# Performance work log

Hardware: AMD Instinct MI355X
Metric: run time of the kernel (lower is better)

The kernel has to match this reference:

```python
import jax, jax.numpy as jnp
import numpy as np

N_NODES = 50000
N_EDGES = 800000
D_IN, D_HID, D_OUT = 128, 128, 64


def setup_inputs() -> dict:
    key = jax.random.key(0)
    ks = jax.random.split(key, 8)
    x = jax.random.normal(ks[0], (N_NODES, D_IN), dtype=jnp.float32)
    edge_index = jax.random.randint(ks[1], (2, N_EDGES), 0, N_NODES, dtype=jnp.int64)
    s1 = 1.0 / np.sqrt(D_IN)
    s2 = 1.0 / np.sqrt(D_HID)
    # PyG SAGEConv: out = lin_l(mean_aggr(x_j)) + lin_r(x_root); bias lives in lin_l
    Wl1 = jax.random.uniform(ks[2], (D_HID, D_IN), jnp.float32, -s1, s1)
    bl1 = jnp.zeros((D_HID,), jnp.float32)
    Wr1 = jax.random.uniform(ks[3], (D_HID, D_IN), jnp.float32, -s1, s1)
    Wl2 = jax.random.uniform(ks[4], (D_OUT, D_HID), jnp.float32, -s2, s2)
    bl2 = jnp.zeros((D_OUT,), jnp.float32)
    Wr2 = jax.random.uniform(ks[5], (D_OUT, D_HID), jnp.float32, -s2, s2)
    return {"x": x, "edge_index": edge_index, "Wl1": Wl1, "bl1": bl1, "Wr1": Wr1,
            "Wl2": Wl2, "bl2": bl2, "Wr2": Wr2}


def _sage_conv(x, src, dst, Wl, bl, Wr):
    # mean aggregation of source-node features onto destination nodes
    msg = x[src]                                              # [E, d]
    agg = jax.ops.segment_sum(msg, dst, num_segments=N_NODES)  # [N, d]
    cnt = jax.ops.segment_sum(jnp.ones((src.shape[0],), x.dtype), dst,
                              num_segments=N_NODES)            # [N]
    mean = agg / jnp.maximum(cnt, 1.0)[:, None]
    return mean @ Wl.T + bl + x @ Wr.T


def reference(x, edge_index, Wl1, bl1, Wr1, Wl2, bl2, Wr2):
    src, dst = edge_index[0], edge_index[1]
    h = jax.nn.relu(_sage_conv(x, src, dst, Wl1, bl1, Wr1))
    h = jax.nn.relu(_sage_conv(h, src, dst, Wl2, bl2, Wr2))
    return jax.nn.log_softmax(h, axis=-1)
```

## Files before the change

kernel.cpp:

```cpp
#include <hip/hip_runtime.h>
#include <cstdint>
#include <cstddef>

#define N_NODES 50000
#define N_EDGES 800000
#define ROWS_PAD 50048
#define ZROW 50000
#define BUCKET_CAP 64

typedef _Float16 f16;
typedef _Float16 f16x2 __attribute__((ext_vector_type(2)));
typedef _Float16 f16x8 __attribute__((ext_vector_type(8)));
typedef float f32x2 __attribute__((ext_vector_type(2)));
typedef float f32x4 __attribute__((ext_vector_type(4)));
typedef unsigned short us4 __attribute__((ext_vector_type(4)));


#define NRANGE 16
#define EPT 16
#define CHUNK (256 * EPT)
#define NCHUNK ((N_EDGES + CHUNK - 1) / CHUNK)
#define NB_FILL (NCHUNK * NRANGE)
#define NB_CX 3125
#define NB_CW 192
#define RANGE_SZ (N_NODES / NRANGE)

__global__ __launch_bounds__(256) void preprocess_kernel(
    const int* __restrict__ edge, int* __restrict__ cnt, unsigned short* __restrict__ bucket,
    const float* __restrict__ x, f16* __restrict__ X16, unsigned char* __restrict__ X8,
    unsigned char* __restrict__ H8,
    const float* __restrict__ Wl1, const float* __restrict__ Wr1,
    const float* __restrict__ Wl2, const float* __restrict__ Wr2,
    f16* __restrict__ Wc1, f16* __restrict__ Wc2) {
  const int b = blockIdx.x;
  const int tid = threadIdx.x;
  if (b < NB_FILL) {
    const int r = b & (NRANGE - 1), chunk = b >> 4;
    const int lo = r * RANGE_SZ, hi = lo + RANGE_SZ;
    const int base = chunk * CHUNK + tid;
    #pragma unroll
    for (int i = 0; i < EPT; ++i) {
      const int e = base + i * 256;
      if (e < N_EDGES) {
        const int dst = edge[N_EDGES + e];
        if (dst >= lo && dst < hi) {
          const int src = edge[e];
          const int pos = atomicAdd(&cnt[dst], 1);
          if (pos < BUCKET_CAP) bucket[(size_t)dst * BUCKET_CAP + pos] = (unsigned short)src;
        }
      }
    }
  } else if (b < NB_FILL + NB_CX) {
    const int idx = (b - NB_FILL) * 256 + tid;
    const int row = idx >> 4, c8 = idx & 15;
    const float4 v0 = *reinterpret_cast<const float4*>(x + (size_t)row * 128 + c8 * 8);
    const float4 v1 = *reinterpret_cast<const float4*>(x + (size_t)row * 128 + c8 * 8 + 4);
    f16x8 o;
    o[0] = (f16)v0.x; o[1] = (f16)v0.y; o[2] = (f16)v0.z; o[3] = (f16)v0.w;
    o[4] = (f16)v1.x; o[5] = (f16)v1.y; o[6] = (f16)v1.z; o[7] = (f16)v1.w;
    *reinterpret_cast<f16x8*>(X16 + (size_t)row * 128 + c8 * 8) = o;
    uint2 p;
    int w = __builtin_amdgcn_cvt_pk_fp8_f32(v0.x, v0.y, 0, false);
    w = __builtin_amdgcn_cvt_pk_fp8_f32(v0.z, v0.w, w, true);
    p.x = (unsigned int)w;
    w = __builtin_amdgcn_cvt_pk_fp8_f32(v1.x, v1.y, 0, false);
    w = __builtin_amdgcn_cvt_pk_fp8_f32(v1.z, v1.w, w, true);
    p.y = (unsigned int)w;
    *reinterpret_cast<uint2*>(X8 + (size_t)row * 128 + c8 * 8) = p;
  } else if (b < NB_FILL + NB_CX + NB_CW) {
    const int idx = (b - NB_FILL - NB_CX) * 256 + tid;
    if (idx < 128 * 256) {
      const int n = idx >> 8, k = idx & 255;
      Wc1[idx] = (f16)((k < 128) ? Wl1[n * 128 + k] : Wr1[n * 128 + (k - 128)]);
    } else {
      const int j = idx - 128 * 256;
      const int n = j >> 8, k = j & 255;
      Wc2[j] = (f16)((k < 128) ? Wl2[n * 128 + k] : Wr2[n * 128 + (k - 128)]);
    }
  } else {
    if (tid < 32)
      reinterpret_cast<unsigned int*>(X8 + (size_t)ZROW * 128)[tid] = 0u;
    else if (tid < 64)
      reinterpret_cast<unsigned int*>(H8 + (size_t)ZROW * 128)[tid - 32] = 0u;
  }
}


__device__ __forceinline__ void aggregate_to_lds(
    const unsigned char* __restrict__ F8, const int* __restrict__ cnt,
    const unsigned short* __restrict__ bucket,
    f16 (*M)[136], int wid, int lane) {
  const int quad = lane >> 4, l16 = lane & 15;
  #pragma unroll 1
  for (int g = 0; g < 2; ++g) {
    const int nb = blockIdx.x * 32 + wid * 8 + g * 4;
    const int node = nb + quad;
    const int dv = (lane < 4) ? cnt[nb + lane] : 0;
    const int dq = __shfl(dv, quad, 64);
    const int dqc = min(dq, BUCKET_CAP);
    int md = max(max(__shfl(dv, 0, 64), __shfl(dv, 1, 64)),
                 max(__shfl(dv, 2, 64), __shfl(dv, 3, 64)));
    md = min(md, BUCKET_CAP);
    const us4 b4 = *reinterpret_cast<const us4*>(bucket + (size_t)node * BUCKET_CAP + l16 * 4);
    float acc[8];
    #pragma unroll
    for (int c = 0; c < 8; ++c) acc[c] = 0.f;
    const unsigned char* Fsrc = F8 + l16 * 8;
    for (int j = 0; j < md; j += 16) {
      uint2 v[16];
      #pragma unroll
      for (int k = 0; k < 16; ++k) {
        const int slot = j + k;
        const int idx = __shfl((int)b4[k & 3], quad * 16 + (slot >> 2), 64);
        const int row = (slot < dqc) ? idx : ZROW;
        v[k] = *reinterpret_cast<const uint2*>(Fsrc + (size_t)row * 128);
      }
      #pragma unroll
      for (int k = 0; k < 16; ++k) {
        const f32x2 f0 = __builtin_amdgcn_cvt_pk_f32_fp8((int)v[k].x, false);
        const f32x2 f1 = __builtin_amdgcn_cvt_pk_f32_fp8((int)v[k].x, true);
        const f32x2 f2 = __builtin_amdgcn_cvt_pk_f32_fp8((int)v[k].y, false);
        const f32x2 f3 = __builtin_amdgcn_cvt_pk_f32_fp8((int)v[k].y, true);
        acc[0] += f0[0]; acc[1] += f0[1]; acc[2] += f1[0]; acc[3] += f1[1];
        acc[4] += f2[0]; acc[5] += f2[1]; acc[6] += f3[0]; acc[7] += f3[1];
      }
    }
    const float inv = 1.0f / (float)(dq > 0 ? dq : 1);
    f16x8 o;
    #pragma unroll
    for (int c = 0; c < 8; ++c) o[c] = (f16)(acc[c] * inv);
    *reinterpret_cast<f16x8*>(&M[wid * 8 + g * 4 + quad][l16 * 8]) = o;
  }
}


__global__ __launch_bounds__(256, 4) void layer1_kernel(
    const f16* __restrict__ X16, const unsigned char* __restrict__ X8,
    const int* __restrict__ cnt, const unsigned short* __restrict__ bucket,
    const f16* __restrict__ Wc, const float* __restrict__ bias,
    f16* __restrict__ H16, unsigned char* __restrict__ H8) {
  __shared__ f16 M[32][136];
  const int wid = threadIdx.x >> 6, lane = threadIdx.x & 63;
  const int quad = lane >> 4, l16 = lane & 15;
  aggregate_to_lds(X8, cnt, bucket, M, wid, lane);
  __syncthreads();
  const int rhalf = wid & 1, nhalf = wid >> 1;
  const int row0 = blockIdx.x * 32 + rhalf * 16;
  f32x4 acc[4];
  #pragma unroll
  for (int t = 0; t < 4; ++t) acc[t] = (f32x4){0.f, 0.f, 0.f, 0.f};
  const f16x8* Wb = reinterpret_cast<const f16x8*>(Wc) + quad;
  const f16* Xrow = X16 + (size_t)(row0 + l16) * 128 + quad * 8;
  #pragma unroll
  for (int s = 0; s < 8; ++s) {
    const f16x8 a = (s < 4)
        ? *reinterpret_cast<const f16x8*>(&M[rhalf * 16 + l16][quad * 8 + s * 32])
        : *reinterpret_cast<const f16x8*>(Xrow + (s - 4) * 32);
    #pragma unroll
    for (int t = 0; t < 4; ++t) {
      const int u = nhalf * 4 + t;
      const f16x8 bb = Wb[(u * 16 + l16) * 32 + s * 4];
      acc[t] = __builtin_amdgcn_mfma_f32_16x16x32_f16(a, bb, acc[t], 0, 0, 0);
    }
  }
  #pragma unroll
  for (int t = 0; t < 4; ++t) {
    const int col = (nhalf * 4 + t) * 16 + l16;
    const float bv = bias[col];
    #pragma unroll
    for (int r = 0; r < 4; ++r) {
      const int row = row0 + quad * 4 + r;
      if (row < N_NODES) {
        const float vv = fmaxf(acc[t][r] + bv, 0.f);
        H16[(size_t)row * 128 + col] = (f16)vv;
        const int p = __builtin_amdgcn_cvt_pk_fp8_f32(vv, vv, 0, false);
        H8[(size_t)row * 128 + col] = (unsigned char)(p & 0xFF);
      }
    }
  }
}


__global__ __launch_bounds__(256, 4) void layer2_kernel(
    const f16* __restrict__ H16, const unsigned char* __restrict__ H8,
    const int* __restrict__ cnt, const unsigned short* __restrict__ bucket,
    const f16* __restrict__ Wc, const float* __restrict__ bias,
    float* __restrict__ out) {
  __shared__ f16 M[32][136];
  __shared__ float PM[4][16], PS[4][16];
  const int wid = threadIdx.x >> 6, lane = threadIdx.x & 63;
  const int quad = lane >> 4, l16 = lane & 15;
  aggregate_to_lds(H8, cnt, bucket, M, wid, lane);
  __syncthreads();
  const int rhalf = wid & 1, nhalf = wid >> 1;
  const int row0 = blockIdx.x * 32 + rhalf * 16;
  f32x4 acc[2];
  #pragma unroll
  for (int t = 0; t < 2; ++t) acc[t] = (f32x4){0.f, 0.f, 0.f, 0.f};
  const f16x8* Wb = reinterpret_cast<const f16x8*>(Wc) + quad;
  const f16* Hrow = H16 + (size_t)(row0 + l16) * 128 + quad * 8;
  #pragma unroll
  for (int s = 0; s < 8; ++s) {
    const f16x8 a = (s < 4)
        ? *reinterpret_cast<const f16x8*>(&M[rhalf * 16 + l16][quad * 8 + s * 32])
        : *reinterpret_cast<const f16x8*>(Hrow + (s - 4) * 32);
    #pragma unroll
    for (int t = 0; t < 2; ++t) {
      const int u = nhalf * 2 + t;
      const f16x8 bb = Wb[(u * 16 + l16) * 32 + s * 4];
      acc[t] = __builtin_amdgcn_mfma_f32_16x16x32_f16(a, bb, acc[t], 0, 0, 0);
    }
  }
  float bv[2];
  #pragma unroll
  for (int t = 0; t < 2; ++t) bv[t] = bias[(nhalf * 2 + t) * 16 + l16];
  float v[4][2], pm[4], ps[4];
  #pragma unroll
  for (int r = 0; r < 4; ++r) {
    #pragma unroll
    for (int t = 0; t < 2; ++t) v[r][t] = fmaxf(acc[t][r] + bv[t], 0.f);
    float m = fmaxf(v[r][0], v[r][1]);
    #pragma unroll
    for (int off = 1; off < 16; off <<= 1) m = fmaxf(m, __shfl_xor(m, off, 64));
    float s = __expf(v[r][0] - m) + __expf(v[r][1] - m);
    #pragma unroll
    for (int off = 1; off < 16; off <<= 1) s += __shfl_xor(s, off, 64);
    pm[r] = m;
    ps[r] = s;
  }
  if (l16 == 0) {
    #pragma unroll
    for (int r = 0; r < 4; ++r) {
      PM[wid][quad * 4 + r] = pm[r];
      PS[wid][quad * 4 + r] = ps[r];
    }
  }
  __syncthreads();
  #pragma unroll
  for (int r = 0; r < 4; ++r) {
    const float m2 = PM[wid ^ 2][quad * 4 + r];
    const float s2 = PS[wid ^ 2][quad * 4 + r];
    const float mt = fmaxf(pm[r], m2);
    const float st = ps[r] * __expf(pm[r] - mt) + s2 * __expf(m2 - mt);
    const float ls = mt + __logf(st);
    const int row = row0 + quad * 4 + r;
    if (row < N_NODES) {
      #pragma unroll
      for (int t = 0; t < 2; ++t)
        out[(size_t)row * 64 + (nhalf * 2 + t) * 16 + l16] = v[r][t] - ls;
    }
  }
}


extern "C" void kernel_launch(void* const* d_in, const int* in_sizes, int n_in,
                              void* d_out, int out_size, void* d_ws, size_t ws_size,
                              hipStream_t stream) {
  const float* x   = (const float*)d_in[0];
  const int* edge  = (const int*)d_in[1];
  const float* Wl1 = (const float*)d_in[2];
  const float* bl1 = (const float*)d_in[3];
  const float* Wr1 = (const float*)d_in[4];
  const float* Wl2 = (const float*)d_in[5];
  const float* bl2 = (const float*)d_in[6];
  const float* Wr2 = (const float*)d_in[7];
  float* out = (float*)d_out;

  char* ws = (char*)d_ws;
  size_t off = 0;
  auto alloc = [&](size_t bytes) -> char* {
    char* p = ws + off;
    off = (off + bytes + 255) & ~(size_t)255;
    return p;
  };
  int* cnt               = (int*)alloc((size_t)ROWS_PAD * 4);
  unsigned short* bucket = (unsigned short*)alloc((size_t)ROWS_PAD * BUCKET_CAP * 2);
  f16* X16           = (f16*)alloc((size_t)ROWS_PAD * 128 * 2);
  f16* H16           = (f16*)alloc((size_t)ROWS_PAD * 128 * 2);
  unsigned char* X8  = (unsigned char*)alloc((size_t)ROWS_PAD * 128);
  unsigned char* H8  = (unsigned char*)alloc((size_t)ROWS_PAD * 128);
  f16* Wc1           = (f16*)alloc((size_t)128 * 256 * 2);
  f16* Wc2           = (f16*)alloc((size_t)64 * 256 * 2);

  hipMemsetAsync(cnt, 0, (size_t)ROWS_PAD * 4, stream);

  preprocess_kernel<<<NB_FILL + NB_CX + NB_CW + 1, 256, 0, stream>>>(
      edge, cnt, bucket, x, X16, X8, H8, Wl1, Wr1, Wl2, Wr2, Wc1, Wc2);

  layer1_kernel<<<ROWS_PAD / 32, 256, 0, stream>>>(X16, X8, cnt, bucket, Wc1, bl1, H16, H8);
  layer2_kernel<<<ROWS_PAD / 32, 256, 0, stream>>>(H16, H8, cnt, bucket, Wc2, bl2, out);
}
```

Measured before the change: 216.7 us.

## Halve rows per block in layer kernels and use nontemporal preprocessing loads

Layer kernels now handle 16 nodes per block instead of 32. Each wave aggregates a single group of 4 nodes, and the MFMA work is split across the four waves by output column tiles, with the layer-2 log-softmax reduced over all four waves. This doubles the grid so there are more independent blocks to hide gather latency and to spread the tail. The cost is more blocks and reloading the weight tiles per block. Preprocessing also switches edge and x loads and the X16/X8 stores to nontemporal builtins to avoid polluting the cache.

After: 232.8 us. 1.07x slower.

```diff
diff --git a/kernel.cpp b/kernel.cpp
--- a/kernel.cpp
+++ b/kernel.cpp
@@ -13,6 +13,8 @@
 typedef _Float16 f16x8 __attribute__((ext_vector_type(8)));
 typedef float f32x2 __attribute__((ext_vector_type(2)));
 typedef float f32x4 __attribute__((ext_vector_type(4)));
+typedef float fx4 __attribute__((ext_vector_type(4)));
+typedef unsigned int u32x2 __attribute__((ext_vector_type(2)));
 typedef unsigned short us4 __attribute__((ext_vector_type(4)));
 
 
@@ -42,9 +44,9 @@
     for (int i = 0; i < EPT; ++i) {
       const int e = base + i * 256;
       if (e < N_EDGES) {
-        const int dst = edge[N_EDGES + e];
+        const int dst = __builtin_nontemporal_load(edge + N_EDGES + e);
         if (dst >= lo && dst < hi) {
-          const int src = edge[e];
+          const int src = __builtin_nontemporal_load(edge + e);
           const int pos = atomicAdd(&cnt[dst], 1);
           if (pos < BUCKET_CAP) bucket[(size_t)dst * BUCKET_CAP + pos] = (unsigned short)src;
         }
@@ -53,20 +55,22 @@
   } else if (b < NB_FILL + NB_CX) {
     const int idx = (b - NB_FILL) * 256 + tid;
     const int row = idx >> 4, c8 = idx & 15;
-    const float4 v0 = *reinterpret_cast<const float4*>(x + (size_t)row * 128 + c8 * 8);
-    const float4 v1 = *reinterpret_cast<const float4*>(x + (size_t)row * 128 + c8 * 8 + 4);
+    const fx4 v0 =
+        __builtin_nontemporal_load(reinterpret_cast<const fx4*>(x + (size_t)row * 128 + c8 * 8));
+    const fx4 v1 = __builtin_nontemporal_load(
+        reinterpret_cast<const fx4*>(x + (size_t)row * 128 + c8 * 8 + 4));
     f16x8 o;
-    o[0] = (f16)v0.x; o[1] = (f16)v0.y; o[2] = (f16)v0.z; o[3] = (f16)v0.w;
-    o[4] = (f16)v1.x; o[5] = (f16)v1.y; o[6] = (f16)v1.z; o[7] = (f16)v1.w;
-    *reinterpret_cast<f16x8*>(X16 + (size_t)row * 128 + c8 * 8) = o;
-    uint2 p;
-    int w = __builtin_amdgcn_cvt_pk_fp8_f32(v0.x, v0.y, 0, false);
-    w = __builtin_amdgcn_cvt_pk_fp8_f32(v0.z, v0.w, w, true);
-    p.x = (unsigned int)w;
-    w = __builtin_amdgcn_cvt_pk_fp8_f32(v1.x, v1.y, 0, false);
-    w = __builtin_amdgcn_cvt_pk_fp8_f32(v1.z, v1.w, w, true);
-    p.y = (unsigned int)w;
-    *reinterpret_cast<uint2*>(X8 + (size_t)row * 128 + c8 * 8) = p;
+    o[0] = (f16)v0[0]; o[1] = (f16)v0[1]; o[2] = (f16)v0[2]; o[3] = (f16)v0[3];
+    o[4] = (f16)v1[0]; o[5] = (f16)v1[1]; o[6] = (f16)v1[2]; o[7] = (f16)v1[3];
+    __builtin_nontemporal_store(o, reinterpret_cast<f16x8*>(X16 + (size_t)row * 128 + c8 * 8));
+    u32x2 p;
+    int w = __builtin_amdgcn_cvt_pk_fp8_f32(v0[0], v0[1], 0, false);
+    w = __builtin_amdgcn_cvt_pk_fp8_f32(v0[2], v0[3], w, true);
+    p[0] = (unsigned int)w;
+    w = __builtin_amdgcn_cvt_pk_fp8_f32(v1[0], v1[1], 0, false);
+    w = __builtin_amdgcn_cvt_pk_fp8_f32(v1[2], v1[3], w, true);
+    p[1] = (unsigned int)w;
+    __builtin_nontemporal_store(p, reinterpret_cast<u32x2*>(X8 + (size_t)row * 128 + c8 * 8));
   } else if (b < NB_FILL + NB_CX + NB_CW) {
     const int idx = (b - NB_FILL - NB_CX) * 256 + tid;
     if (idx < 128 * 256) {
@@ -86,51 +90,48 @@
 }
 
 
-__device__ __forceinline__ void aggregate_to_lds(
+__device__ __forceinline__ void aggregate4_to_lds(
     const unsigned char* __restrict__ F8, const int* __restrict__ cnt,
     const unsigned short* __restrict__ bucket,
     f16 (*M)[136], int wid, int lane) {
   const int quad = lane >> 4, l16 = lane & 15;
-  #pragma unroll 1
-  for (int g = 0; g < 2; ++g) {
-    const int nb = blockIdx.x * 32 + wid * 8 + g * 4;
-    const int node = nb + quad;
-    const int dv = (lane < 4) ? cnt[nb + lane] : 0;
-    const int dq = __shfl(dv, quad, 64);
-    const int dqc = min(dq, BUCKET_CAP);
-    int md = max(max(__shfl(dv, 0, 64), __shfl(dv, 1, 64)),
-                 max(__shfl(dv, 2, 64), __shfl(dv, 3, 64)));
-    md = min(md, BUCKET_CAP);
-    const us4 b4 = *reinterpret_cast<const us4*>(bucket + (size_t)node * BUCKET_CAP + l16 * 4);
-    float acc[8];
-    #pragma unroll
-    for (int c = 0; c < 8; ++c) acc[c] = 0.f;
-    const unsigned char* Fsrc = F8 + l16 * 8;
-    for (int j = 0; j < md; j += 16) {
-      uint2 v[16];
-      #pragma unroll
-      for (int k = 0; k < 16; ++k) {
-        const int slot = j + k;
-        const int idx = __shfl((int)b4[k & 3], quad * 16 + (slot >> 2), 64);
-        const int row = (slot < dqc) ? idx : ZROW;
-        v[k] = *reinterpret_cast<const uint2*>(Fsrc + (size_t)row * 128);
-      }
-      #pragma unroll
-      for (int k = 0; k < 16; ++k) {
-        const f32x2 f0 = __builtin_amdgcn_cvt_pk_f32_fp8((int)v[k].x, false);
-        const f32x2 f1 = __builtin_amdgcn_cvt_pk_f32_fp8((int)v[k].x, true);
-        const f32x2 f2 = __builtin_amdgcn_cvt_pk_f32_fp8((int)v[k].y, false);
-        const f32x2 f3 = __builtin_amdgcn_cvt_pk_f32_fp8((int)v[k].y, true);
-        acc[0] += f0[0]; acc[1] += f0[1]; acc[2] += f1[0]; acc[3] += f1[1];
-        acc[4] += f2[0]; acc[5] += f2[1]; acc[6] += f3[0]; acc[7] += f3[1];
-      }
-    }
-    const float inv = 1.0f / (float)(dq > 0 ? dq : 1);
-    f16x8 o;
-    #pragma unroll
-    for (int c = 0; c < 8; ++c) o[c] = (f16)(acc[c] * inv);
-    *reinterpret_cast<f16x8*>(&M[wid * 8 + g * 4 + quad][l16 * 8]) = o;
-  }
+  const int nb = blockIdx.x * 16 + wid * 4;
+  const int node = nb + quad;
+  const int dv = (lane < 4) ? cnt[nb + lane] : 0;
+  const int dq = __shfl(dv, quad, 64);
+  const int dqc = min(dq, BUCKET_CAP);
+  int md = max(max(__shfl(dv, 0, 64), __shfl(dv, 1, 64)),
+               max(__shfl(dv, 2, 64), __shfl(dv, 3, 64)));
+  md = min(md, BUCKET_CAP);
+  const us4 b4 = *reinterpret_cast<const us4*>(bucket + (size_t)node * BUCKET_CAP + l16 * 4);
+  float acc[8];
+  #pragma unroll
+  for (int c = 0; c < 8; ++c) acc[c] = 0.f;
+  const unsigned char* Fsrc = F8 + l16 * 8;
+  for (int j = 0; j < md; j += 16) {
+    u32x2 v[16];
+    #pragma unroll
+    for (int k = 0; k < 16; ++k) {
+      const int slot = j + k;
+      const int idx = __shfl((int)b4[k & 3], quad * 16 + (slot >> 2), 64);
+      const int row = (slot < dqc) ? idx : ZROW;
+      v[k] = *reinterpret_cast<const u32x2*>(Fsrc + (size_t)row * 128);
+    }
+    #pragma unroll
+    for (int k = 0; k < 16; ++k) {
+      const f32x2 f0 = __builtin_amdgcn_cvt_pk_f32_fp8((int)v[k][0], false);
+      const f32x2 f1 = __builtin_amdgcn_cvt_pk_f32_fp8((int)v[k][0], true);
+      const f32x2 f2 = __builtin_amdgcn_cvt_pk_f32_fp8((int)v[k][1], false);
+      const f32x2 f3 = __builtin_amdgcn_cvt_pk_f32_fp8((int)v[k][1], true);
+      acc[0] += f0[0]; acc[1] += f0[1]; acc[2] += f1[0]; acc[3] += f1[1];
+      acc[4] += f2[0]; acc[5] += f2[1]; acc[6] += f3[0]; acc[7] += f3[1];
+    }
+  }
+  const float inv = 1.0f / (float)(dq > 0 ? dq : 1);
+  f16x8 o;
+  #pragma unroll
+  for (int c = 0; c < 8; ++c) o[c] = (f16)(acc[c] * inv);
+  *reinterpret_cast<f16x8*>(&M[wid * 4 + quad][l16 * 8]) = o;
 }
 
 
@@ -139,33 +140,32 @@
     const int* __restrict__ cnt, const unsigned short* __restrict__ bucket,
     const f16* __restrict__ Wc, const float* __restrict__ bias,
     f16* __restrict__ H16, unsigned char* __restrict__ H8) {
-  __shared__ f16 M[32][136];
+  __shared__ f16 M[16][136];
   const int wid = threadIdx.x >> 6, lane = threadIdx.x & 63;
   const int quad = lane >> 4, l16 = lane & 15;
-  aggregate_to_lds(X8, cnt, bucket, M, wid, lane);
+  aggregate4_to_lds(X8, cnt, bucket, M, wid, lane);
   __syncthreads();
-  const int rhalf = wid & 1, nhalf = wid >> 1;
-  const int row0 = blockIdx.x * 32 + rhalf * 16;
-  f32x4 acc[4];
-  #pragma unroll
-  for (int t = 0; t < 4; ++t) acc[t] = (f32x4){0.f, 0.f, 0.f, 0.f};
+  const int row0 = blockIdx.x * 16;
+  f32x4 acc[2];
+  #pragma unroll
+  for (int t = 0; t < 2; ++t) acc[t] = (f32x4){0.f, 0.f, 0.f, 0.f};
   const f16x8* Wb = reinterpret_cast<const f16x8*>(Wc) + quad;
   const f16* Xrow = X16 + (size_t)(row0 + l16) * 128 + quad * 8;
   #pragma unroll
   for (int s = 0; s < 8; ++s) {
     const f16x8 a = (s < 4)
-        ? *reinterpret_cast<const f16x8*>(&M[rhalf * 16 + l16][quad * 8 + s * 32])
+        ? *reinterpret_cast<const f16x8*>(&M[l16][quad * 8 + s * 32])
         : *reinterpret_cast<const f16x8*>(Xrow + (s - 4) * 32);
     #pragma unroll
-    for (int t = 0; t < 4; ++t) {
-      const int u = nhalf * 4 + t;
+    for (int t = 0; t < 2; ++t) {
+      const int u = wid * 2 + t;
       const f16x8 bb = Wb[(u * 16 + l16) * 32 + s * 4];
       acc[t] = __builtin_amdgcn_mfma_f32_16x16x32_f16(a, bb, acc[t], 0, 0, 0);
     }
   }
   #pragma unroll
-  for (int t = 0; t < 4; ++t) {
-    const int col = (nhalf * 4 + t) * 16 + l16;
+  for (int t = 0; t < 2; ++t) {
+    const int col = (wid * 2 + t) * 16 + l16;
     const float bv = bias[col];
     #pragma unroll
     for (int r = 0; r < 4; ++r) {
@@ -186,43 +186,33 @@
     const int* __restrict__ cnt, const unsigned short* __restrict__ bucket,
     const f16* __restrict__ Wc, const float* __restrict__ bias,
     float* __restrict__ out) {
-  __shared__ f16 M[32][136];
+  __shared__ f16 M[16][136];
   __shared__ float PM[4][16], PS[4][16];
   const int wid = threadIdx.x >> 6, lane = threadIdx.x & 63;
   const int quad = lane >> 4, l16 = lane & 15;
-  aggregate_to_lds(H8, cnt, bucket, M, wid, lane);
+  aggregate4_to_lds(H8, cnt, bucket, M, wid, lane);
   __syncthreads();
-  const int rhalf = wid & 1, nhalf = wid >> 1;
-  const int row0 = blockIdx.x * 32 + rhalf * 16;
-  f32x4 acc[2];
-  #pragma unroll
-  for (int t = 0; t < 2; ++t) acc[t] = (f32x4){0.f, 0.f, 0.f, 0.f};
+  const int row0 = blockIdx.x * 16;
+  f32x4 acc = (f32x4){0.f, 0.f, 0.f, 0.f};
   const f16x8* Wb = reinterpret_cast<const f16x8*>(Wc) + quad;
   const f16* Hrow = H16 + (size_t)(row0 + l16) * 128 + quad * 8;
   #pragma unroll
   for (int s = 0; s < 8; ++s) {
     const f16x8 a = (s < 4)
-        ? *reinterpret_cast<const f16x8*>(&M[rhalf * 16 + l16][quad * 8 + s * 32])
+        ? *reinterpret_cast<const f16x8*>(&M[l16][quad * 8 + s * 32])
         : *reinterpret_cast<const f16x8*>(Hrow + (s - 4) * 32);
-    #pragma unroll
-    for (int t = 0; t < 2; ++t) {
-      const int u = nhalf * 2 + t;
-      const f16x8 bb = Wb[(u * 16 + l16) * 32 + s * 4];
-      acc[t] = __builtin_amdgcn_mfma_f32_16x16x32_f16(a, bb, acc[t], 0, 0, 0);
-    }
-  }
-  float bv[2];
-  #pragma unroll
-  for (int t = 0; t < 2; ++t) bv[t] = bias[(nhalf * 2 + t) * 16 + l16];
-  float v[4][2], pm[4], ps[4];
+    const f16x8 bb = Wb[(wid * 16 + l16) * 32 + s * 4];
+    acc = __builtin_amdgcn_mfma_f32_16x16x32_f16(a, bb, acc, 0, 0, 0);
+  }
+  const float bv = bias[wid * 16 + l16];
+  float v[4], pm[4], ps[4];
   #pragma unroll
   for (int r = 0; r < 4; ++r) {
-    #pragma unroll
-    for (int t = 0; t < 2; ++t) v[r][t] = fmaxf(acc[t][r] + bv[t], 0.f);
-    float m = fmaxf(v[r][0], v[r][1]);
+    v[r] = fmaxf(acc[r] + bv, 0.f);
+    float m = v[r];
     #pragma unroll
     for (int off = 1; off < 16; off <<= 1) m = fmaxf(m, __shfl_xor(m, off, 64));
-    float s = __expf(v[r][0] - m) + __expf(v[r][1] - m);
+    float s = __expf(v[r] - m);
     #pragma unroll
     for (int off = 1; off < 16; off <<= 1) s += __shfl_xor(s, off, 64);
     pm[r] = m;
@@ -238,17 +228,15 @@
   __syncthreads();
   #pragma unroll
   for (int r = 0; r < 4; ++r) {
-    const float m2 = PM[wid ^ 2][quad * 4 + r];
-    const float s2 = PS[wid ^ 2][quad * 4 + r];
-    const float mt = fmaxf(pm[r], m2);
-    const float st = ps[r] * __expf(pm[r] - mt) + s2 * __expf(m2 - mt);
+    const int idx = quad * 4 + r;
+    const float m0 = PM[0][idx], m1 = PM[1][idx], m2 = PM[2][idx], m3 = PM[3][idx];
+    const float mt = fmaxf(fmaxf(m0, m1), fmaxf(m2, m3));
+    const float st = PS[0][idx] * __expf(m0 - mt) + PS[1][idx] * __expf(m1 - mt) +
+                     PS[2][idx] * __expf(m2 - mt) + PS[3][idx] * __expf(m3 - mt);
     const float ls = mt + __logf(st);
-    const int row = row0 + quad * 4 + r;
-    if (row < N_NODES) {
-      #pragma unroll
-      for (int t = 0; t < 2; ++t)
-        out[(size_t)row * 64 + (nhalf * 2 + t) * 16 + l16] = v[r][t] - ls;
-    }
+    const int row = row0 + idx;
+    if (row < N_NODES)
+      out[(size_t)row * 64 + wid * 16 + l16] = v[r] - ls;
   }
 }
 
@@ -287,6 +275,6 @@
   preprocess_kernel<<<NB_FILL + NB_CX + NB_CW + 1, 256, 0, stream>>>(
       edge, cnt, bucket, x, X16, X8, H8, Wl1, Wr1, Wl2, Wr2, Wc1, Wc2);
 
-  layer1_kernel<<<ROWS_PAD / 32, 256, 0, stream>>>(X16, X8, cnt, bucket, Wc1, bl1, H16, H8);
-  layer2_kernel<<<ROWS_PAD / 32, 256, 0, stream>>>(H16, H8, cnt, bucket, Wc2, bl2, out);
-}
+  layer1_kernel<<<ROWS_PAD / 16, 256, 0, stream>>>(X16, X8, cnt, bucket, Wc1, bl1, H16, H8);
+  layer2_kernel<<<ROWS_PAD / 16, 256, 0, stream>>>(H16, H8, cnt, bucket, Wc2, bl2, out);
+}
```

## Drop fp16 feature copies and read root features from fp8 buffers

Applied to the files above, without the earlier changes.

Removes the X16 and H16 half-precision copies, so the root-term operand of each layer's MFMA is loaded from the existing fp8 buffers and decoded in registers. The root-row loads are issued before aggregation so they overlap with the gather. The aggregation gather loop is unrolled to 32 outstanding loads instead of 16. This cuts global write and read traffic for the fp16 copies. In exchange the root term loses precision (fp8 instead of fp16) and register pressure rises from the larger gather unroll.

Result: slower. 232.5 us (+7.3%).

```diff
diff --git a/kernel.cpp b/kernel.cpp
--- a/kernel.cpp
+++ b/kernel.cpp
@@ -13,6 +13,8 @@
 typedef _Float16 f16x8 __attribute__((ext_vector_type(8)));
 typedef float f32x2 __attribute__((ext_vector_type(2)));
 typedef float f32x4 __attribute__((ext_vector_type(4)));
+typedef float fx4 __attribute__((ext_vector_type(4)));
+typedef unsigned int u32x2 __attribute__((ext_vector_type(2)));
 typedef unsigned short us4 __attribute__((ext_vector_type(4)));
 
 
@@ -27,8 +29,7 @@
 
 __global__ __launch_bounds__(256) void preprocess_kernel(
     const int* __restrict__ edge, int* __restrict__ cnt, unsigned short* __restrict__ bucket,
-    const float* __restrict__ x, f16* __restrict__ X16, unsigned char* __restrict__ X8,
-    unsigned char* __restrict__ H8,
+    const float* __restrict__ x, unsigned char* __restrict__ X8, unsigned char* __restrict__ H8,
     const float* __restrict__ Wl1, const float* __restrict__ Wr1,
     const float* __restrict__ Wl2, const float* __restrict__ Wr2,
     f16* __restrict__ Wc1, f16* __restrict__ Wc2) {
@@ -53,20 +54,16 @@
   } else if (b < NB_FILL + NB_CX) {
     const int idx = (b - NB_FILL) * 256 + tid;
     const int row = idx >> 4, c8 = idx & 15;
-    const float4 v0 = *reinterpret_cast<const float4*>(x + (size_t)row * 128 + c8 * 8);
-    const float4 v1 = *reinterpret_cast<const float4*>(x + (size_t)row * 128 + c8 * 8 + 4);
-    f16x8 o;
-    o[0] = (f16)v0.x; o[1] = (f16)v0.y; o[2] = (f16)v0.z; o[3] = (f16)v0.w;
-    o[4] = (f16)v1.x; o[5] = (f16)v1.y; o[6] = (f16)v1.z; o[7] = (f16)v1.w;
-    *reinterpret_cast<f16x8*>(X16 + (size_t)row * 128 + c8 * 8) = o;
-    uint2 p;
-    int w = __builtin_amdgcn_cvt_pk_fp8_f32(v0.x, v0.y, 0, false);
-    w = __builtin_amdgcn_cvt_pk_fp8_f32(v0.z, v0.w, w, true);
-    p.x = (unsigned int)w;
-    w = __builtin_amdgcn_cvt_pk_fp8_f32(v1.x, v1.y, 0, false);
-    w = __builtin_amdgcn_cvt_pk_fp8_f32(v1.z, v1.w, w, true);
-    p.y = (unsigned int)w;
-    *reinterpret_cast<uint2*>(X8 + (size_t)row * 128 + c8 * 8) = p;
+    const fx4 v0 = *reinterpret_cast<const fx4*>(x + (size_t)row * 128 + c8 * 8);
+    const fx4 v1 = *reinterpret_cast<const fx4*>(x + (size_t)row * 128 + c8 * 8 + 4);
+    u32x2 p;
+    int w = __builtin_amdgcn_cvt_pk_fp8_f32(v0[0], v0[1], 0, false);
+    w = __builtin_amdgcn_cvt_pk_fp8_f32(v0[2], v0[3], w, true);
+    p[0] = (unsigned int)w;
+    w = __builtin_amdgcn_cvt_pk_fp8_f32(v1[0], v1[1], 0, false);
+    w = __builtin_amdgcn_cvt_pk_fp8_f32(v1[2], v1[3], w, true);
+    p[1] = (unsigned int)w;
+    *reinterpret_cast<u32x2*>(X8 + (size_t)row * 128 + c8 * 8) = p;
   } else if (b < NB_FILL + NB_CX + NB_CW) {
     const int idx = (b - NB_FILL - NB_CX) * 256 + tid;
     if (idx < 128 * 256) {
@@ -83,6 +80,17 @@
     else if (tid < 64)
       reinterpret_cast<unsigned int*>(H8 + (size_t)ZROW * 128)[tid - 32] = 0u;
   }
+}
+
+__device__ __forceinline__ f16x8 decode8(u32x2 v) {
+  const f32x2 f0 = __builtin_amdgcn_cvt_pk_f32_fp8((int)v[0], false);
+  const f32x2 f1 = __builtin_amdgcn_cvt_pk_f32_fp8((int)v[0], true);
+  const f32x2 f2 = __builtin_amdgcn_cvt_pk_f32_fp8((int)v[1], false);
+  const f32x2 f3 = __builtin_amdgcn_cvt_pk_f32_fp8((int)v[1], true);
+  f16x8 a;
+  a[0] = (f16)f0[0]; a[1] = (f16)f0[1]; a[2] = (f16)f1[0]; a[3] = (f16)f1[1];
+  a[4] = (f16)f2[0]; a[5] = (f16)f2[1]; a[6] = (f16)f3[0]; a[7] = (f16)f3[1];
+  return a;
 }
 
 
@@ -106,21 +114,21 @@
     #pragma unroll
     for (int c = 0; c < 8; ++c) acc[c] = 0.f;
     const unsigned char* Fsrc = F8 + l16 * 8;
-    for (int j = 0; j < md; j += 16) {
-      uint2 v[16];
+    for (int j = 0; j < md; j += 32) {
+      u32x2 v[32];
       #pragma unroll
-      for (int k = 0; k < 16; ++k) {
+      for (int k = 0; k < 32; ++k) {
         const int slot = j + k;
         const int idx = __shfl((int)b4[k & 3], quad * 16 + (slot >> 2), 64);
         const int row = (slot < dqc) ? idx : ZROW;
-        v[k] = *reinterpret_cast<const uint2*>(Fsrc + (size_t)row * 128);
+        v[k] = *reinterpret_cast<const u32x2*>(Fsrc + (size_t)row * 128);
       }
       #pragma unroll
-      for (int k = 0; k < 16; ++k) {
-        const f32x2 f0 = __builtin_amdgcn_cvt_pk_f32_fp8((int)v[k].x, false);
-        const f32x2 f1 = __builtin_amdgcn_cvt_pk_f32_fp8((int)v[k].x, true);
-        const f32x2 f2 = __builtin_amdgcn_cvt_pk_f32_fp8((int)v[k].y, false);
-        const f32x2 f3 = __builtin_amdgcn_cvt_pk_f32_fp8((int)v[k].y, true);
+      for (int k = 0; k < 32; ++k) {
+        const f32x2 f0 = __builtin_amdgcn_cvt_pk_f32_fp8((int)v[k][0], false);
+        const f32x2 f1 = __builtin_amdgcn_cvt_pk_f32_fp8((int)v[k][0], true);
+        const f32x2 f2 = __builtin_amdgcn_cvt_pk_f32_fp8((int)v[k][1], false);
+        const f32x2 f3 = __builtin_amdgcn_cvt_pk_f32_fp8((int)v[k][1], true);
         acc[0] += f0[0]; acc[1] += f0[1]; acc[2] += f1[0]; acc[3] += f1[1];
         acc[4] += f2[0]; acc[5] += f2[1]; acc[6] += f3[0]; acc[7] += f3[1];
       }
@@ -135,27 +143,31 @@
 
 
 __global__ __launch_bounds__(256, 4) void layer1_kernel(
-    const f16* __restrict__ X16, const unsigned char* __restrict__ X8,
+    const unsigned char* __restrict__ X8,
     const int* __restrict__ cnt, const unsigned short* __restrict__ bucket,
     const f16* __restrict__ Wc, const float* __restrict__ bias,
-    f16* __restrict__ H16, unsigned char* __restrict__ H8) {
+    unsigned char* __restrict__ H8) {
   __shared__ f16 M[32][136];
   const int wid = threadIdx.x >> 6, lane = threadIdx.x & 63;
   const int quad = lane >> 4, l16 = lane & 15;
+  const int rhalf = wid & 1, nhalf = wid >> 1;
+  const int row0 = blockIdx.x * 32 + rhalf * 16;
+  const unsigned char* Xrow = X8 + (size_t)(row0 + l16) * 128 + quad * 8;
+  u32x2 rr[4];
+  #pragma unroll
+  for (int s2 = 0; s2 < 4; ++s2)
+    rr[s2] = *reinterpret_cast<const u32x2*>(Xrow + s2 * 32);
   aggregate_to_lds(X8, cnt, bucket, M, wid, lane);
   __syncthreads();
-  const int rhalf = wid & 1, nhalf = wid >> 1;
-  const int row0 = blockIdx.x * 32 + rhalf * 16;
   f32x4 acc[4];
   #pragma unroll
   for (int t = 0; t < 4; ++t) acc[t] = (f32x4){0.f, 0.f, 0.f, 0.f};
   const f16x8* Wb = reinterpret_cast<const f16x8*>(Wc) + quad;
-  const f16* Xrow = X16 + (size_t)(row0 + l16) * 128 + quad * 8;
   #pragma unroll
   for (int s = 0; s < 8; ++s) {
     const f16x8 a = (s < 4)
         ? *reinterpret_cast<const f16x8*>(&M[rhalf * 16 + l16][quad * 8 + s * 32])
-        : *reinterpret_cast<const f16x8*>(Xrow + (s - 4) * 32);
+        : decode8(rr[s - 4]);
     #pragma unroll
     for (int t = 0; t < 4; ++t) {
       const int u = nhalf * 4 + t;
@@ -172,7 +184,6 @@
       const int row = row0 + quad * 4 + r;
       if (row < N_NODES) {
         const float vv = fmaxf(acc[t][r] + bv, 0.f);
-        H16[(size_t)row * 128 + col] = (f16)vv;
         const int p = __builtin_amdgcn_cvt_pk_fp8_f32(vv, vv, 0, false);
         H8[(size_t)row * 128 + col] = (unsigned char)(p & 0xFF);
       }
@@ -182,7 +193,7 @@
 
 
 __global__ __launch_bounds__(256, 4) void layer2_kernel(
-    const f16* __restrict__ H16, const unsigned char* __restrict__ H8,
+    const unsigned char* __restrict__ H8,
     const int* __restrict__ cnt, const unsigned short* __restrict__ bucket,
     const f16* __restrict__ Wc, const float* __restrict__ bias,
     float* __restrict__ out) {
@@ -190,20 +201,24 @@
   __shared__ float PM[4][16], PS[4][16];
   const int wid = threadIdx.x >> 6, lane = threadIdx.x & 63;
   const int quad = lane >> 4, l16 = lane & 15;
+  const int rhalf = wid & 1, nhalf = wid >> 1;
+  const int row0 = blockIdx.x * 32 + rhalf * 16;
+  const unsigned char* Hrow = H8 + (size_t)(row0 + l16) * 128 + quad * 8;
+  u32x2 rr[4];
+  #pragma unroll
+  for (int s2 = 0; s2 < 4; ++s2)
+    rr[s2] = *reinterpret_cast<const u32x2*>(Hrow + s2 * 32);
   aggregate_to_lds(H8, cnt, bucket, M, wid, lane);
   __syncthreads();
-  const int rhalf = wid & 1, nhalf = wid >> 1;
-  const int row0 = blockIdx.x * 32 + rhalf * 16;
   f32x4 acc[2];
   #pragma unroll
   for (int t = 0; t < 2; ++t) acc[t] = (f32x4){0.f, 0.f, 0.f, 0.f};
   const f16x8* Wb = reinterpret_cast<const f16x8*>(Wc) + quad;
-  const f16* Hrow = H16 + (size_t)(row0 + l16) * 128 + quad * 8;
   #pragma unroll
   for (int s = 0; s < 8; ++s) {
     const f16x8 a = (s < 4)
         ? *reinterpret_cast<const f16x8*>(&M[rhalf * 16 + l16][quad * 8 + s * 32])
-        : *reinterpret_cast<const f16x8*>(Hrow + (s - 4) * 32);
+        : decode8(rr[s - 4]);
     #pragma unroll
     for (int t = 0; t < 2; ++t) {
       const int u = nhalf * 2 + t;
@@ -275,8 +290,6 @@
   };
   int* cnt               = (int*)alloc((size_t)ROWS_PAD * 4);
   unsigned short* bucket = (unsigned short*)alloc((size_t)ROWS_PAD * BUCKET_CAP * 2);
-  f16* X16           = (f16*)alloc((size_t)ROWS_PAD * 128 * 2);
-  f16* H16           = (f16*)alloc((size_t)ROWS_PAD * 128 * 2);
   unsigned char* X8  = (unsigned char*)alloc((size_t)ROWS_PAD * 128);
   unsigned char* H8  = (unsigned char*)alloc((size_t)ROWS_PAD * 128);
   f16* Wc1           = (f16*)alloc((size_t)128 * 256 * 2);
@@ -285,8 +298,8 @@
   hipMemsetAsync(cnt, 0, (size_t)ROWS_PAD * 4, stream);
 
   preprocess_kernel<<<NB_FILL + NB_CX + NB_CW + 1, 256, 0, stream>>>(
-      edge, cnt, bucket, x, X16, X8, H8, Wl1, Wr1, Wl2, Wr2, Wc1, Wc2);
-
-  layer1_kernel<<<ROWS_PAD / 32, 256, 0, stream>>>(X16, X8, cnt, bucket, Wc1, bl1, H16, H8);
-  layer2_kernel<<<ROWS_PAD / 32, 256, 0, stream>>>(H16, H8, cnt, bucket, Wc2, bl2, out);
-}
+      edge, cnt, bucket, x, X8, H8, Wl1, Wr1, Wl2, Wr2, Wc1, Wc2);
+
+  layer1_kernel<<<ROWS_PAD / 32, 256, 0, stream>>>(X8, cnt, bucket, Wc1, bl1, H8);
+  layer2_kernel<<<ROWS_PAD / 32, 256, 0, stream>>>(H8, cnt, bucket, Wc2, bl2, out);
+}
```
